# Kernel optimization log

Hardware: AMD Instinct MI355X
Metric: run time of the kernel (lower is better)

The kernel has to match this reference:

```python
import jax, jax.numpy as jnp
from jax import lax
import numpy as np

SCALE, K_UP = 2, 5


def conv2d(x, w, pad=0, dil=1):
    return lax.conv_general_dilated(x, w, (1, 1), [(pad, pad), (pad, pad)],
                                    rhs_dilation=(dil, dil),
                                    dimension_numbers=('NCHW', 'OIHW', 'NCHW'))


def cbr(x, w, g, b, pad=0, relu=True):
    # Conv (no bias) + BatchNorm (eval: running_mean=0, running_var=1, eps=1e-5) + optional ReLU
    x = conv2d(x, w, pad)
    x = x * (g / jnp.sqrt(1.0 + 1e-5))[None, :, None, None] + b[None, :, None, None]
    return jnp.maximum(x, 0.0) if relu else x


def resize_bilinear_ac(x, ho, wo):
    # bilinear interpolation, align_corners=True (matches F.interpolate)
    B, C, H, W = x.shape
    ys = jnp.linspace(0.0, H - 1.0, ho)
    xs = jnp.linspace(0.0, W - 1.0, wo)
    y0 = jnp.floor(ys).astype(jnp.int32); y1 = jnp.minimum(y0 + 1, H - 1)
    x0 = jnp.floor(xs).astype(jnp.int32); x1 = jnp.minimum(x0 + 1, W - 1)
    wy = (ys - y0).astype(x.dtype)
    wx = (xs - x0).astype(x.dtype)
    top = x[:, :, y0, :]
    bot = x[:, :, y1, :]
    v = top * (1.0 - wy)[None, None, :, None] + bot * wy[None, None, :, None]
    return v[:, :, :, x0] * (1.0 - wx) + v[:, :, :, x1] * wx


def setup_inputs() -> dict:
    key = jax.random.key(0)
    ks = jax.random.split(key, 10)
    B, CH, CL, H, W = 4, 256, 128, 64, 64
    CMID, CO, IC, KENC = 64, 128, 64, 3

    def wgt(k, shape):
        fan = int(np.prod(shape[1:]))
        return (jax.random.normal(k, shape, jnp.float32) / np.sqrt(fan)).astype(jnp.float32)

    d = {}
    d['x_h'] = jax.random.normal(ks[0], (B, CH, H, W), jnp.float32)
    d['x_l'] = jax.random.normal(ks[1], (B, CL, H * SCALE, W * SCALE), jnp.float32)
    d['w_reduce'] = wgt(ks[2], (IC, CH, 3, 3)); d['g_reduce'] = jnp.ones(IC); d['b_reduce'] = jnp.zeros(IC)
    d['w1'] = wgt(ks[3], (CMID, CH, 1, 1)); d['g1'] = jnp.ones(CMID); d['b1'] = jnp.zeros(CMID)
    d['w2'] = wgt(ks[4], (CMID, CL, 1, 1)); d['g2'] = jnp.ones(CMID); d['b2'] = jnp.zeros(CMID)
    d['w_enc'] = wgt(ks[5], (K_UP * K_UP, 2 * CMID, KENC, KENC)); d['g_enc'] = jnp.ones(K_UP * K_UP); d['b_enc'] = jnp.zeros(K_UP * K_UP)
    d['w_out1'] = wgt(ks[6], (CO, IC + CL, 3, 3)); d['g_out1'] = jnp.ones(CO); d['b_out1'] = jnp.zeros(CO)
    d['w_out2'] = wgt(ks[7], (CO, CO, 1, 1)); d['g_out2'] = jnp.ones(CO); d['b_out2'] = jnp.zeros(CO)
    return d


def reference(x_h, x_l, w_reduce, g_reduce, b_reduce, w1, g1, b1, w2, g2, b2,
              w_enc, g_enc, b_enc, w_out1, g_out1, b_out1, w_out2, g_out2, b_out2):
    b, c, h, w = x_h.shape
    h_, w_ = h * SCALE, w * SCALE
    # content encoder -> per-pixel reassembly kernels
    x1 = resize_bilinear_ac(cbr(x_h, w1, g1, b1), h_, w_)          # [b, cmid, h_, w_]
    x2 = cbr(x_l, w2, g2, b2)                                       # [b, cmid, h_, w_]
    Wm = cbr(jnp.concatenate([x1, x2], axis=1), w_enc, g_enc, b_enc, pad=1, relu=False)
    Wm = jax.nn.softmax(Wm, axis=1)                                  # [b, k_up^2, h_, w_]
    # reduced high-level features, upsampled
    xr = cbr(x_h, w_reduce, g_reduce, b_reduce, pad=1)               # [b, ic, h, w]
    xu = resize_bilinear_ac(xr, h_, w_)                              # [b, ic, h_, w_]
    # CARAFE-style reassembly: unfold(k=5, dilation=2, pad=4) expressed as
    # 25 shifted windows of the zero-padded map -> no k^2-blown buffer.
    pad = (K_UP // 2) * SCALE
    xp = jnp.pad(xu, ((0, 0), (0, 0), (pad, pad), (pad, pad)))
    X = jnp.zeros_like(xu)
    for i in range(K_UP):
        for j in range(K_UP):
            win = xp[:, :, i * SCALE:i * SCALE + h_, j * SCALE:j * SCALE + w_]
            X = X + Wm[:, i * K_UP + j][:, None] * win
    y = jnp.concatenate([X, x_l], axis=1)
    y = cbr(y, w_out1, g_out1, b_out1, pad=1)
    y = cbr(y, w_out2, g_out2, b_out2)
    return y
```

## Files before the change

### kernel.cpp

```cpp
#include <hip/hip_runtime.h>
#include <math.h>

#define BNS 0.99999500003749981f

typedef short          bf16x8  __attribute__((ext_vector_type(8)));
typedef float          f32x4   __attribute__((ext_vector_type(4)));
typedef unsigned short u16x8   __attribute__((ext_vector_type(8)));
typedef unsigned short u16x4   __attribute__((ext_vector_type(4)));
typedef unsigned short ushort_t;

__device__ inline ushort_t f2b(float f) {
    union { float f; unsigned int u; } x; x.f = f;
    unsigned int u = x.u;
    unsigned int r = (u + 0x7FFFu + ((u >> 16) & 1u)) >> 16;
    return (ushort_t)r;
}
__device__ inline float b2f(ushort_t s) {
    union { unsigned int u; float f; } x; x.u = ((unsigned int)s) << 16;
    return x.f;
}

__device__ inline void glds16(const ushort_t* gp, void* lp) {
    __builtin_amdgcn_global_load_lds(
        (const __attribute__((address_space(1))) unsigned int*)gp,
        (__attribute__((address_space(3))) unsigned int*)lp, 16, 0, 0);
}

template<int N, bool LG0>
__device__ __forceinline__ void wait_v() {
    if constexpr (LG0) {
        if constexpr (N == 0) asm volatile("s_waitcnt vmcnt(0) lgkmcnt(0)" ::: "memory");
        if constexpr (N == 3) asm volatile("s_waitcnt vmcnt(3) lgkmcnt(0)" ::: "memory");
        if constexpr (N == 4) asm volatile("s_waitcnt vmcnt(4) lgkmcnt(0)" ::: "memory");
        if constexpr (N == 5) asm volatile("s_waitcnt vmcnt(5) lgkmcnt(0)" ::: "memory");
        if constexpr (N == 6) asm volatile("s_waitcnt vmcnt(6) lgkmcnt(0)" ::: "memory");
    } else {
        if constexpr (N == 0) asm volatile("s_waitcnt vmcnt(0)" ::: "memory");
        if constexpr (N == 3) asm volatile("s_waitcnt vmcnt(3)" ::: "memory");
        if constexpr (N == 4) asm volatile("s_waitcnt vmcnt(4)" ::: "memory");
        if constexpr (N == 5) asm volatile("s_waitcnt vmcnt(5)" ::: "memory");
        if constexpr (N == 6) asm volatile("s_waitcnt vmcnt(6)" ::: "memory");
    }
}

#define E_BWR   0u
#define E_BW1   147456u
#define E_BW2   163840u
#define E_BWE   172032u
#define E_BWO1  208896u
#define E_BWO2  430080u
#define E_ZP    446464u
#define OFF_R1  524288u
#define OFF_R4  4718592u
#define OFF_R2  8912896u
#define OFF_R3  9961472u
#define OFF_R6  11010048u
#define OFF_R5  13107200u


__device__ inline void wseg3(int idx, const float* src, ushort_t* dst,
                             int TAPS, int COT, int CIT, int CO_real) {
    int kt  = idx / (COT * 32);
    int r   = idx - kt * (COT * 32);
    int q   = r / (COT * 8);
    int r2  = r - q * (COT * 8);
    int co  = r2 >> 3;
    int e   = r2 & 7;
    int KCT = CIT >> 5;
    int tap = kt / KCT, j = kt - tap * KCT;
    int ci  = j * 32 + q * 8 + e;
    float v = (co < CO_real) ? src[((size_t)co * CIT + ci) * TAPS + tap] : 0.f;
    dst[idx] = f2b(v);
}

__global__ __launch_bounds__(256)
void prep_weights(const float* wr, const float* w1, const float* w2,
                  const float* we, const float* wo1, const float* wo2,
                  ushort_t* ws0)
{
    int idx = blockIdx.x * 256 + threadIdx.x;
    const int n0 = 9*64*256;
    const int n1 = 64*256;
    const int n2 = 64*128;
    const int n3 = 9*32*128;
    const int n4 = 9*128*192;
    const int n5 = 128*128;
    if (idx < n0) { wseg3(idx, wr,  ws0 + E_BWR,  9, 64, 256, 64);  return; } idx -= n0;
    if (idx < n1) { wseg3(idx, w1,  ws0 + E_BW1,  1, 64, 256, 64);  return; } idx -= n1;
    if (idx < n2) { wseg3(idx, w2,  ws0 + E_BW2,  1, 64, 128, 64);  return; } idx -= n2;
    if (idx < n3) { wseg3(idx, we,  ws0 + E_BWE,  9, 32, 128, 25);  return; } idx -= n3;
    if (idx < n4) { wseg3(idx, wo1, ws0 + E_BWO1, 9, 128, 192, 128); return; } idx -= n4;
    if (idx < n5) { wseg3(idx, wo2, ws0 + E_BWO2, 1, 128, 128, 128); return; } idx -= n5;
    if (idx < 32768) ws0[E_ZP + idx] = 0;
}

__global__ __launch_bounds__(256)
void nchw2t16(const float* __restrict__ in, ushort_t* __restrict__ out,
              int C, int LHW, int npx)
{
    int px = blockIdx.x * 256 + threadIdx.x;
    if (px >= npx) return;
    int HW = 1 << LHW;
    int b = px >> LHW, phw = px & (HW - 1);
    const float* src = in + (size_t)b * C * HW + phw;
    unsigned base = (unsigned)(px >> 4) * (C * 16) + (unsigned)(px & 15) * 8;
    for (int c0 = 0; c0 < C; c0 += 8) {
        u16x8 o;
#pragma unroll
        for (int j = 0; j < 8; j++) o[j] = f2b(src[(size_t)(c0 + j) * HW]);
        *reinterpret_cast<u16x8*>(out + base + (c0 >> 3) * 128) = o;
    }
}

template<int TAPS, int BM, int CIA, int CIB, int COT, int BN, int G, int EPI>
__global__ __launch_bounds__(256)
void conv_lds(const ushort_t* __restrict__ ws0,
              unsigned offA, unsigned offB, unsigned offW,
              const float* __restrict__ g, const float* __restrict__ bia,
              int COclamp, void* __restrict__ outp,
              int H, int LHW, int relu)
{
    constexpr int KCA = CIA / 32, KCB = CIB / 32;
    constexpr int KCT = KCA + KCB;
    constexpr int NW  = (TAPS == 9) ? 3 : G;
    constexpr int ACP = (TAPS == 9) ? 1 : G;
    constexpr int NPH = (TAPS == 9) ? 3 * KCT : KCT / G;
    constexpr int MF = BM / 32, NF = BN / 32;
    constexpr int ACHUNK = BM / 16;
    constexpr int A4 = ACP * ACHUNK / 4;
    constexpr int WUNIT = BN / 16;
    constexpr int TWU = NW * WUNIT;
    constexpr int W4 = (TWU + 3) / 4;
    constexpr int SS = A4 + W4;
    constexpr int WOFF = ACP * BM * 64;
    constexpr int ZS   = WOFF + NW * BN * 64;
    constexpr int BUF  = ZS + 16;
    constexpr int LBN3 = (BN == 128) ? 10 : (BN == 64) ? 9 : 8;
    __shared__ __align__(16) char lds[2 * BUF];

    const unsigned nx = gridDim.x, ox = blockIdx.x;
    const unsigned qq = nx >> 3, xcd = ox & 7, k0 = ox >> 3;
    const unsigned bx = xcd * qq + k0;
    const int co_blk = blockIdx.y * BN;

    const int tid = threadIdx.x, w = tid >> 6, lane = tid & 63;
    const int l15 = lane & 15, lhi = lane >> 4;
    const int wpx = (w & 1) * (BM / 2), cw0 = (w >> 1) * (BN / 2);
    const int yb = (int)(bx & (unsigned)(H - 1));
    const unsigned pxc0 = bx * ACHUNK;

    if (tid < 8) *(unsigned*)(lds + (tid >> 2) * BUF + ZS + (tid & 3) * 4) = 0u;

    int aA[3][MF];
#pragma unroll
    for (int dxi = 0; dxi < 3; ++dxi) {
        const int dx = dxi - 1;
#pragma unroll
        for (int mf = 0; mf < MF; ++mf) {
            int pr = wpx + mf * 16 + l15 + dx;
            bool ok = (TAPS == 1) ? true : (pr >= 0 && pr < BM);
            aA[dxi][mf] = ok ? (((pr >> 4) << 10) + (lhi << 8) + ((pr & 15) << 4))
                             : (ZS - ((TAPS == 9) ? 0 : 0));
            if (TAPS == 9 && !ok) aA[dxi][mf] = ZS;
        }
    }
    int wA[NF];
#pragma unroll
    for (int nf = 0; nf < NF; ++nf)
        wA[nf] = (lhi * BN + cw0 + nf * 16 + l15) * 16;

    f32x4 acc[NF][MF];
#pragma unroll
    for (int nf = 0; nf < NF; ++nf)
#pragma unroll
        for (int mf = 0; mf < MF; ++mf)
            acc[nf][mf] = (f32x4){0.f, 0.f, 0.f, 0.f};

    auto stage = [&](int p, int bsel) {
        char* lb = lds + bsel * BUF;
        if constexpr (TAPS == 9) {
            const int dyi = p / KCT, kc = p - dyi * KCT;
            const int dy = dyi - 1;
            const bool isA = (kc < KCA);
            const int kcs = isA ? kc : kc - KCA;
            const int CI  = isA ? CIA : CIB;
            const unsigned offS = isA ? offA : offB;
            const bool rowv = (yb + dy >= 0) && (yb + dy < H);
#pragma unroll
            for (int i = 0; i < A4; ++i) {
                int u = i * 4 + w;
                unsigned s = rowv
                    ? offS + (unsigned)((int)pxc0 + dy * ACHUNK + u) * (unsigned)(CI * 16)
                           + (unsigned)(kcs * 512) + (unsigned)(lane * 8)
                    : E_ZP + (unsigned)(lane * 8);
                glds16(ws0 + s, lb + u * 1024);
            }
#pragma unroll
            for (int i = 0; i < W4; ++i) {
                int t3 = (i * 4 + w) % TWU;
                int tl = t3 / WUNIT, uu = t3 - tl * WUNIT;
                unsigned wsrc = offW + (unsigned)((dyi * 3 + tl) * KCT + kc)
                                       * (unsigned)(COT * 32);
                int el  = uu * 512 + lane * 8;
                int q   = el >> LBN3;
                int col = (el & ((1 << LBN3) - 1)) >> 3;
                glds16(ws0 + wsrc + q * (COT * 8) + (co_blk + col) * 8,
                       lb + WOFF + tl * (BN * 64) + uu * 1024);
            }
        } else {
#pragma unroll
            for (int i = 0; i < A4; ++i) {
                int lin = i * 4 + w;
                int gc = lin / ACHUNK, u = lin - gc * ACHUNK;
                unsigned s = offA + (unsigned)(pxc0 + u) * (unsigned)(CIA * 16)
                           + (unsigned)((p * G + gc) * 512) + (unsigned)(lane * 8);
                glds16(ws0 + s, lb + gc * (BM * 64) + u * 1024);
            }
#pragma unroll
            for (int i = 0; i < W4; ++i) {
                int t3 = (i * 4 + w) % TWU;
                int tl = t3 / WUNIT, uu = t3 - tl * WUNIT;
                unsigned wsrc = offW + (unsigned)(p * G + tl) * (unsigned)(COT * 32);
                int el  = uu * 512 + lane * 8;
                int q   = el >> LBN3;
                int col = (el & ((1 << LBN3) - 1)) >> 3;
                glds16(ws0 + wsrc + q * (COT * 8) + (co_blk + col) * 8,
                       lb + WOFF + tl * (BN * 64) + uu * 1024);
            }
        }
    };

    auto step = [&](int p, int bsel) {
        const char* lb = lds + bsel * BUF;
#pragma unroll
        for (int t = 0; t < NW; ++t) {
            const int dxi = (TAPS == 9) ? t : 1;
            const char* ab = lb + ((TAPS == 9) ? 0 : t * (BM * 64));
            bf16x8 af[MF], wf[NF];
#pragma unroll
            for (int mf = 0; mf < MF; ++mf)
                af[mf] = *reinterpret_cast<const bf16x8*>(ab + aA[dxi][mf]);
#pragma unroll
            for (int nf = 0; nf < NF; ++nf)
                wf[nf] = *reinterpret_cast<const bf16x8*>(
                    lb + WOFF + t * (BN * 64) + wA[nf]);
#pragma unroll
            for (int nf = 0; nf < NF; ++nf)
#pragma unroll
                for (int mf = 0; mf < MF; ++mf)
                    acc[nf][mf] = __builtin_amdgcn_mfma_f32_16x16x32_bf16(
                        wf[nf], af[mf], acc[nf][mf], 0, 0, 0);
        }
    };

    stage(0, 0);
#pragma unroll
    for (int p = 0; p < NPH; ++p) {
        if (p + 1 < NPH) stage(p + 1, (p + 1) & 1);
        if (p == 0) { if (p + 1 < NPH) wait_v<SS, true >(); else wait_v<0, true >(); }
        else        { if (p + 1 < NPH) wait_v<SS, false>(); else wait_v<0, false>(); }
        __builtin_amdgcn_s_barrier();
        __builtin_amdgcn_sched_barrier(0);
        step(p, p & 1);
        __builtin_amdgcn_sched_barrier(0);
        if (p + 1 < NPH) __builtin_amdgcn_s_barrier();
    }

    if constexpr (EPI == 0) {
        ushort_t* o1 = (ushort_t*)outp;
#pragma unroll
        for (int nf = 0; nf < NF; ++nf) {
            const int cg = co_blk + cw0 + nf * 16 + (lhi << 2);
            float sc[4], bi[4];
#pragma unroll
            for (int r = 0; r < 4; r++) {
                int c = min(cg + r, COclamp - 1);
                sc[r] = g[c] * BNS; bi[r] = bia[c];
            }
#pragma unroll
            for (int mf = 0; mf < MF; ++mf) {
                f32x4 a = acc[nf][mf];
                u16x4 ov;
#pragma unroll
                for (int r = 0; r < 4; r++) {
                    float v = fmaf(a[r], sc[r], bi[r]);
                    if (relu) v = fmaxf(v, 0.f);
                    ov[r] = f2b(v);
                }
                int px = (int)bx * BM + wpx + mf * 16 + l15;
                unsigned off = (unsigned)(px >> 4) * (COT * 16)
                             + (unsigned)(cg >> 3) * 128
                             + (unsigned)(px & 15) * 8 + (unsigned)(cg & 7);
                *reinterpret_cast<u16x4*>(o1 + off) = ov;
            }
        }
    } else if constexpr (EPI == 1) {
        float* o1 = (float*)outp;
        const int HW = 1 << LHW;
#pragma unroll
        for (int nf = 0; nf < NF; ++nf) {
            const int cg = co_blk + cw0 + nf * 16 + (lhi << 2);
            float sc[4], bi[4];
#pragma unroll
            for (int r = 0; r < 4; r++) {
                int c = min(cg + r, COclamp - 1);
                sc[r] = g[c] * BNS; bi[r] = bia[c];
            }
#pragma unroll
            for (int mf = 0; mf < MF; ++mf) {
                int px = (int)bx * BM + wpx + mf * 16 + l15;
                int b = px >> LHW, phw = px & (HW - 1);
#pragma unroll
                for (int r = 0; r < 4; r++) {
                    float v = fmaf(acc[nf][mf][r], sc[r], bi[r]);
                    if (relu) v = fmaxf(v, 0.f);
                    o1[((size_t)(b * COT + cg + r)) * HW + phw] = v;
                }
            }
        }
    } else {
        __syncthreads();
        float* sf = (float*)lds;
#pragma unroll
        for (int mf = 0; mf < MF; ++mf) {
            const int cg = cw0 + (lhi << 2);
            int pxl = wpx + mf * 16 + l15;
            f32x4 a = acc[0][mf];
#pragma unroll
            for (int r = 0; r < 4; r++) {
                int c = min(cg + r, COclamp - 1);
                sf[(cg + r) * 136 + pxl] = fmaf(a[r], g[c] * BNS, bia[c]);
            }
        }
        __syncthreads();
        if (tid < BM) {
            int gpx = (int)bx * BM + tid;
            float v[25];
#pragma unroll
            for (int c = 0; c < 25; ++c) v[c] = sf[c * 136 + tid];
            float m = v[0];
#pragma unroll
            for (int c = 1; c < 25; ++c) m = fmaxf(m, v[c]);
            float s = 0.f;
#pragma unroll
            for (int c = 0; c < 25; ++c) { v[c] = __expf(v[c] - m); s += v[c]; }
            float inv = 1.f / s;
            ushort_t* o1 = (ushort_t*)outp;
            unsigned base = (unsigned)(gpx >> 4) * (COT * 16) + (unsigned)(gpx & 15) * 8;
#pragma unroll
            for (int q = 0; q < 3; ++q) {
                u16x8 ov;
#pragma unroll
                for (int k = 0; k < 8; k++) ov[k] = f2b(v[q * 8 + k] * inv);
                *reinterpret_cast<u16x8*>(o1 + base + q * 128) = ov;
            }
            o1[base + 384] = f2b(v[24] * inv);
        }
    }
}

__global__ __launch_bounds__(256)
void resize2x_t16(const ushort_t* __restrict__ in, ushort_t* __restrict__ out)
{
    int t = blockIdx.x * 256 + threadIdx.x;
    int cg = t & 7;
    int opx = t >> 3;
    int xo = opx & 127;
    int rest = opx >> 7;
    int yo = rest & 127;
    int b  = rest >> 7;
    float fy = (float)yo * 63.f / 127.f;
    float fx = (float)xo * 63.f / 127.f;
    int y0 = (int)fy, x0 = (int)fx;
    float wy = fy - (float)y0, wx = fx - (float)x0;
    int y1 = min(y0 + 1, 63), x1 = min(x0 + 1, 63);
    int qb = b * 4096;
#define RD(Y, X) (*reinterpret_cast<const bf16x8*>(in + \
    (unsigned)(((qb + (Y) * 64 + (X)) >> 4) * 1024) + cg * 128 + ((qb + (Y) * 64 + (X)) & 15) * 8))
    bf16x8 v00 = RD(y0, x0), v01 = RD(y0, x1), v10 = RD(y1, x0), v11 = RD(y1, x1);
#undef RD
    u16x8 o;
#pragma unroll
    for (int k = 0; k < 8; k++) {
        float l = b2f((ushort_t)v00[k]) * (1.f - wy) + b2f((ushort_t)v10[k]) * wy;
        float r = b2f((ushort_t)v01[k]) * (1.f - wy) + b2f((ushort_t)v11[k]) * wy;
        o[k] = f2b(l * (1.f - wx) + r * wx);
    }
    *reinterpret_cast<u16x8*>(out + (unsigned)(opx >> 4) * 1024 + cg * 128 + (opx & 15) * 8) = o;
}

__global__ __launch_bounds__(256)
void carafe25(const ushort_t* __restrict__ wm, const ushort_t* __restrict__ xu,
              ushort_t* __restrict__ out)
{
    int t = blockIdx.x * 256 + threadIdx.x;
    int cg = t & 7;
    int px = t >> 3;
    int x = px & 127;
    int y = (px >> 7) & 127;
    const ushort_t* wp = wm + (unsigned)(px >> 4) * 512 + (px & 15) * 8;
    u16x8 r0 = *reinterpret_cast<const u16x8*>(wp);
    u16x8 r1 = *reinterpret_cast<const u16x8*>(wp + 128);
    u16x8 r2 = *reinterpret_cast<const u16x8*>(wp + 256);
    float v[25];
#pragma unroll
    for (int k = 0; k < 8; k++) v[k]      = b2f(r0[k]);
#pragma unroll
    for (int k = 0; k < 8; k++) v[8 + k]  = b2f(r1[k]);
#pragma unroll
    for (int k = 0; k < 8; k++) v[16 + k] = b2f(r2[k]);
    v[24] = b2f(wp[384]);

    float acc[8];
#pragma unroll
    for (int k = 0; k < 8; k++) acc[k] = 0.f;
#pragma unroll
    for (int i = 0; i < 5; i++) {
        int yy = y + 2 * i - 4;
#pragma unroll
        for (int j = 0; j < 5; j++) {
            int xx = x + 2 * j - 4;
            if (yy >= 0 && yy < 128 && xx >= 0 && xx < 128) {
                int q = px + (2 * i - 4) * 128 + (2 * j - 4);
                bf16x8 xv = *reinterpret_cast<const bf16x8*>(
                    xu + (unsigned)(q >> 4) * 1024 + cg * 128 + (q & 15) * 8);
                float wv = v[i * 5 + j];
#pragma unroll
                for (int k = 0; k < 8; k++)
                    acc[k] = fmaf(wv, b2f((ushort_t)xv[k]), acc[k]);
            }
        }
    }
    u16x8 o;
#pragma unroll
    for (int k = 0; k < 8; k++) o[k] = f2b(acc[k]);
    *reinterpret_cast<u16x8*>(out + (unsigned)(px >> 4) * 1024 + cg * 128 + (px & 15) * 8) = o;
}

extern "C" void kernel_launch(void* const* d_in, const int* in_sizes, int n_in,
                              void* d_out, int out_size, void* d_ws, size_t ws_size,
                              hipStream_t stream)
{
    const float* x_h      = (const float*)d_in[0];
    const float* x_l      = (const float*)d_in[1];
    const float* w_reduce = (const float*)d_in[2];
    const float* g_reduce = (const float*)d_in[3];
    const float* b_reduce = (const float*)d_in[4];
    const float* w1       = (const float*)d_in[5];
    const float* g1       = (const float*)d_in[6];
    const float* b1       = (const float*)d_in[7];
    const float* w2       = (const float*)d_in[8];
    const float* g2       = (const float*)d_in[9];
    const float* b2       = (const float*)d_in[10];
    const float* w_enc    = (const float*)d_in[11];
    const float* g_enc    = (const float*)d_in[12];
    const float* b_enc    = (const float*)d_in[13];
    const float* w_out1   = (const float*)d_in[14];
    const float* g_out1   = (const float*)d_in[15];
    const float* b_out1   = (const float*)d_in[16];
    const float* w_out2   = (const float*)d_in[17];
    const float* g_out2   = (const float*)d_in[18];
    const float* b_out2   = (const float*)d_in[19];

    ushort_t* ws0 = (ushort_t*)d_ws;

    const unsigned oXHC = OFF_R1;
    const unsigned oC1  = OFF_R2;
    const unsigned oXR  = OFF_R3;
    const unsigned oX1  = OFF_R4;
    const unsigned oXLC = OFF_R5;
    const unsigned oX2  = OFF_R1;
    const unsigned oWM  = OFF_R6;
    const unsigned oXU  = OFF_R4;
    const unsigned oXB  = OFF_R1;
    const unsigned oY1  = OFF_R4;

    prep_weights<<<1872, 256, 0, stream>>>(w_reduce, w1, w2, w_enc, w_out1, w_out2, ws0);
    nchw2t16<<<64, 256, 0, stream>>>(x_h, ws0 + oXHC, 256, 12, 16384);
    conv_lds<1, 64, 256, 0, 64, 32, 2, 0><<<dim3(256, 2), 256, 0, stream>>>(
        ws0, oXHC, 0u, E_BW1, g1, b1, 64, ws0 + oC1, 64, 12, 1);
    conv_lds<9, 64, 256, 0, 64, 32, 1, 0><<<dim3(256, 2), 256, 0, stream>>>(
        ws0, oXHC, 0u, E_BWR, g_reduce, b_reduce, 64, ws0 + oXR, 64, 12, 1);
    resize2x_t16<<<2048, 256, 0, stream>>>(ws0 + oC1, ws0 + oX1);
    nchw2t16<<<256, 256, 0, stream>>>(x_l, ws0 + oXLC, 128, 14, 65536);
    conv_lds<1, 128, 128, 0, 64, 32, 2, 0><<<dim3(512, 2), 256, 0, stream>>>(
        ws0, oXLC, 0u, E_BW2, g2, b2, 64, ws0 + oX2, 128, 14, 1);
    conv_lds<9, 128, 64, 64, 32, 32, 1, 2><<<dim3(512, 1), 256, 0, stream>>>(
        ws0, oX1, oX2, E_BWE, g_enc, b_enc, 25, ws0 + oWM, 128, 14, 0);
    resize2x_t16<<<2048, 256, 0, stream>>>(ws0 + oXR, ws0 + oXU);
    carafe25<<<2048, 256, 0, stream>>>(ws0 + oWM, ws0 + oXU, ws0 + oXB);
    conv_lds<9, 128, 64, 128, 128, 64, 1, 0><<<dim3(512, 2), 256, 0, stream>>>(
        ws0, oXB, oXLC, E_BWO1, g_out1, b_out1, 128, ws0 + oY1, 128, 14, 1);
    conv_lds<1, 128, 128, 0, 128, 64, 2, 1><<<dim3(512, 2), 256, 0, stream>>>(
        ws0, oY1, 0u, E_BWO2, g_out2, b_out2, 128, d_out, 128, 14, 1);
}
```

Measured before the change: 155.4 us.

## Merge prep kernels, widen conv output tiles, add 3-stage pipeline and MFMA priority

Fuses the weight-prep kernel and both NCHW-to-tiled input conversion kernels into one launch. Generalizes the conv kernel's wave layout (WSX) so a block covers all output channels (BN 64/128, grid.y = 1), which stops input tiles being loaded twice. Adds an optional 3-deep LDS pipeline with matching vmcnt waits, and raises wave priority around the MFMA loop. The cost is more LDS and registers per block, which may lower occupancy, and half as many blocks on some convs.

After: 135.6 us. -12.7%, faster.

```diff
diff --git a/kernel.cpp b/kernel.cpp
--- a/kernel.cpp
+++ b/kernel.cpp
@@ -28,18 +28,19 @@
 
 template<int N, bool LG0>
 __device__ __forceinline__ void wait_v() {
+    static_assert(N >= 0 && N <= 16, "vmcnt literal table");
     if constexpr (LG0) {
-        if constexpr (N == 0) asm volatile("s_waitcnt vmcnt(0) lgkmcnt(0)" ::: "memory");
-        if constexpr (N == 3) asm volatile("s_waitcnt vmcnt(3) lgkmcnt(0)" ::: "memory");
-        if constexpr (N == 4) asm volatile("s_waitcnt vmcnt(4) lgkmcnt(0)" ::: "memory");
-        if constexpr (N == 5) asm volatile("s_waitcnt vmcnt(5) lgkmcnt(0)" ::: "memory");
-        if constexpr (N == 6) asm volatile("s_waitcnt vmcnt(6) lgkmcnt(0)" ::: "memory");
+        if constexpr (N == 0)  asm volatile("s_waitcnt vmcnt(0) lgkmcnt(0)" ::: "memory");
+        if constexpr (N == 3)  asm volatile("s_waitcnt vmcnt(3) lgkmcnt(0)" ::: "memory");
+        if constexpr (N == 4)  asm volatile("s_waitcnt vmcnt(4) lgkmcnt(0)" ::: "memory");
+        if constexpr (N == 6)  asm volatile("s_waitcnt vmcnt(6) lgkmcnt(0)" ::: "memory");
+        if constexpr (N == 8)  asm volatile("s_waitcnt vmcnt(8) lgkmcnt(0)" ::: "memory");
     } else {
-        if constexpr (N == 0) asm volatile("s_waitcnt vmcnt(0)" ::: "memory");
-        if constexpr (N == 3) asm volatile("s_waitcnt vmcnt(3)" ::: "memory");
-        if constexpr (N == 4) asm volatile("s_waitcnt vmcnt(4)" ::: "memory");
-        if constexpr (N == 5) asm volatile("s_waitcnt vmcnt(5)" ::: "memory");
-        if constexpr (N == 6) asm volatile("s_waitcnt vmcnt(6)" ::: "memory");
+        if constexpr (N == 0)  asm volatile("s_waitcnt vmcnt(0)" ::: "memory");
+        if constexpr (N == 3)  asm volatile("s_waitcnt vmcnt(3)" ::: "memory");
+        if constexpr (N == 4)  asm volatile("s_waitcnt vmcnt(4)" ::: "memory");
+        if constexpr (N == 6)  asm volatile("s_waitcnt vmcnt(6)" ::: "memory");
+        if constexpr (N == 8)  asm volatile("s_waitcnt vmcnt(8)" ::: "memory");
     }
 }
 
@@ -73,32 +74,9 @@
     dst[idx] = f2b(v);
 }
 
-__global__ __launch_bounds__(256)
-void prep_weights(const float* wr, const float* w1, const float* w2,
-                  const float* we, const float* wo1, const float* wo2,
-                  ushort_t* ws0)
-{
-    int idx = blockIdx.x * 256 + threadIdx.x;
-    const int n0 = 9*64*256;
-    const int n1 = 64*256;
-    const int n2 = 64*128;
-    const int n3 = 9*32*128;
-    const int n4 = 9*128*192;
-    const int n5 = 128*128;
-    if (idx < n0) { wseg3(idx, wr,  ws0 + E_BWR,  9, 64, 256, 64);  return; } idx -= n0;
-    if (idx < n1) { wseg3(idx, w1,  ws0 + E_BW1,  1, 64, 256, 64);  return; } idx -= n1;
-    if (idx < n2) { wseg3(idx, w2,  ws0 + E_BW2,  1, 64, 128, 64);  return; } idx -= n2;
-    if (idx < n3) { wseg3(idx, we,  ws0 + E_BWE,  9, 32, 128, 25);  return; } idx -= n3;
-    if (idx < n4) { wseg3(idx, wo1, ws0 + E_BWO1, 9, 128, 192, 128); return; } idx -= n4;
-    if (idx < n5) { wseg3(idx, wo2, ws0 + E_BWO2, 1, 128, 128, 128); return; } idx -= n5;
-    if (idx < 32768) ws0[E_ZP + idx] = 0;
-}
-
-__global__ __launch_bounds__(256)
-void nchw2t16(const float* __restrict__ in, ushort_t* __restrict__ out,
-              int C, int LHW, int npx)
-{
-    int px = blockIdx.x * 256 + threadIdx.x;
+__device__ inline void cvt_t16(const float* __restrict__ in,
+                               ushort_t* __restrict__ out,
+                               int C, int LHW, int px, int npx) {
     if (px >= npx) return;
     int HW = 1 << LHW;
     int b = px >> LHW, phw = px & (HW - 1);
@@ -112,7 +90,38 @@
     }
 }
 
-template<int TAPS, int BM, int CIA, int CIB, int COT, int BN, int G, int EPI>
+__global__ __launch_bounds__(256)
+void prep_all(const float* wr, const float* w1, const float* w2,
+              const float* we, const float* wo1, const float* wo2,
+              const float* xh, const float* xl, ushort_t* ws0)
+{
+    int bx = blockIdx.x;
+    int tid = threadIdx.x;
+    if (bx < 1872) {
+        int idx = bx * 256 + tid;
+        const int n0 = 9*64*256;
+        const int n1 = 64*256;
+        const int n2 = 64*128;
+        const int n3 = 9*32*128;
+        const int n4 = 9*128*192;
+        const int n5 = 128*128;
+        if (idx < n0) { wseg3(idx, wr,  ws0 + E_BWR,  9, 64, 256, 64);  return; } idx -= n0;
+        if (idx < n1) { wseg3(idx, w1,  ws0 + E_BW1,  1, 64, 256, 64);  return; } idx -= n1;
+        if (idx < n2) { wseg3(idx, w2,  ws0 + E_BW2,  1, 64, 128, 64);  return; } idx -= n2;
+        if (idx < n3) { wseg3(idx, we,  ws0 + E_BWE,  9, 32, 128, 25);  return; } idx -= n3;
+        if (idx < n4) { wseg3(idx, wo1, ws0 + E_BWO1, 9, 128, 192, 128); return; } idx -= n4;
+        if (idx < n5) { wseg3(idx, wo2, ws0 + E_BWO2, 1, 128, 128, 128); return; } idx -= n5;
+        if (idx < 32768) ws0[E_ZP + idx] = 0;
+        return;
+    }
+    bx -= 1872;
+    if (bx < 64) { cvt_t16(xh, ws0 + OFF_R1, 256, 12, bx * 256 + tid, 16384); return; }
+    bx -= 64;
+    cvt_t16(xl, ws0 + OFF_R5, 128, 14, bx * 256 + tid, 65536);
+}
+
+template<int TAPS, int BM, int CIA, int CIB, int COT, int BN, int G,
+         int WSX, int DEP, int EPI>
 __global__ __launch_bounds__(256)
 void conv_lds(const ushort_t* __restrict__ ws0,
               unsigned offA, unsigned offB, unsigned offW,
@@ -125,9 +134,11 @@
     constexpr int NW  = (TAPS == 9) ? 3 : G;
     constexpr int ACP = (TAPS == 9) ? 1 : G;
     constexpr int NPH = (TAPS == 9) ? 3 * KCT : KCT / G;
-    constexpr int MF = BM / 32, NF = BN / 32;
+    constexpr int WSY = 4 / WSX;
+    constexpr int MF = BM / WSX / 16;
+    constexpr int NF = BN / WSY / 16;
     constexpr int ACHUNK = BM / 16;
-    constexpr int A4 = ACP * ACHUNK / 4;
+    constexpr int A4 = (ACP * ACHUNK + 3) / 4;
     constexpr int WUNIT = BN / 16;
     constexpr int TWU = NW * WUNIT;
     constexpr int W4 = (TWU + 3) / 4;
@@ -136,7 +147,7 @@
     constexpr int ZS   = WOFF + NW * BN * 64;
     constexpr int BUF  = ZS + 16;
     constexpr int LBN3 = (BN == 128) ? 10 : (BN == 64) ? 9 : 8;
-    __shared__ __align__(16) char lds[2 * BUF];
+    __shared__ __align__(16) char lds[DEP * BUF];
 
     const unsigned nx = gridDim.x, ox = blockIdx.x;
     const unsigned qq = nx >> 3, xcd = ox & 7, k0 = ox >> 3;
@@ -145,11 +156,12 @@
 
     const int tid = threadIdx.x, w = tid >> 6, lane = tid & 63;
     const int l15 = lane & 15, lhi = lane >> 4;
-    const int wpx = (w & 1) * (BM / 2), cw0 = (w >> 1) * (BN / 2);
+    const int wpx = (w % WSX) * (BM / WSX);
+    const int cw0 = (w / WSX) * (BN / WSY);
     const int yb = (int)(bx & (unsigned)(H - 1));
     const unsigned pxc0 = bx * ACHUNK;
 
-    if (tid < 8) *(unsigned*)(lds + (tid >> 2) * BUF + ZS + (tid & 3) * 4) = 0u;
+    if (tid < 4 * DEP) *(unsigned*)(lds + (tid >> 2) * BUF + ZS + (tid & 3) * 4) = 0u;
 
     int aA[3][MF];
 #pragma unroll
@@ -159,9 +171,7 @@
         for (int mf = 0; mf < MF; ++mf) {
             int pr = wpx + mf * 16 + l15 + dx;
             bool ok = (TAPS == 1) ? true : (pr >= 0 && pr < BM);
-            aA[dxi][mf] = ok ? (((pr >> 4) << 10) + (lhi << 8) + ((pr & 15) << 4))
-                             : (ZS - ((TAPS == 9) ? 0 : 0));
-            if (TAPS == 9 && !ok) aA[dxi][mf] = ZS;
+            aA[dxi][mf] = ok ? (((pr >> 4) << 10) + (lhi << 8) + ((pr & 15) << 4)) : ZS;
         }
     }
     int wA[NF];
@@ -188,7 +198,7 @@
             const bool rowv = (yb + dy >= 0) && (yb + dy < H);
 #pragma unroll
             for (int i = 0; i < A4; ++i) {
-                int u = i * 4 + w;
+                int u = (i * 4 + w) % ACHUNK;
                 unsigned s = rowv
                     ? offS + (unsigned)((int)pxc0 + dy * ACHUNK + u) * (unsigned)(CI * 16)
                            + (unsigned)(kcs * 512) + (unsigned)(lane * 8)
@@ -210,7 +220,7 @@
         } else {
 #pragma unroll
             for (int i = 0; i < A4; ++i) {
-                int lin = i * 4 + w;
+                int lin = (i * 4 + w) % (ACP * ACHUNK);
                 int gc = lin / ACHUNK, u = lin - gc * ACHUNK;
                 unsigned s = offA + (unsigned)(pxc0 + u) * (unsigned)(CIA * 16)
                            + (unsigned)((p * G + gc) * 512) + (unsigned)(lane * 8);
@@ -232,6 +242,7 @@
 
     auto step = [&](int p, int bsel) {
         const char* lb = lds + bsel * BUF;
+        __builtin_amdgcn_s_setprio(1);
 #pragma unroll
         for (int t = 0; t < NW; ++t) {
             const int dxi = (TAPS == 9) ? t : 1;
@@ -251,17 +262,31 @@
                     acc[nf][mf] = __builtin_amdgcn_mfma_f32_16x16x32_bf16(
                         wf[nf], af[mf], acc[nf][mf], 0, 0, 0);
         }
+        __builtin_amdgcn_s_setprio(0);
     };
 
     stage(0, 0);
+    if constexpr (DEP == 3) { if (1 < NPH) stage(1, 1); }
 #pragma unroll
     for (int p = 0; p < NPH; ++p) {
-        if (p + 1 < NPH) stage(p + 1, (p + 1) & 1);
-        if (p == 0) { if (p + 1 < NPH) wait_v<SS, true >(); else wait_v<0, true >(); }
-        else        { if (p + 1 < NPH) wait_v<SS, false>(); else wait_v<0, false>(); }
+        if (p + DEP - 1 < NPH) stage(p + DEP - 1, (p + DEP - 1) % DEP);
+        if constexpr (DEP == 3) {
+            if (p == 0) {
+                if (p + 2 < NPH)      wait_v<2 * SS, true >();
+                else if (p + 1 < NPH) wait_v<SS,     true >();
+                else                  wait_v<0,      true >();
+            } else {
+                if (p + 2 < NPH)      wait_v<2 * SS, false>();
+                else if (p + 1 < NPH) wait_v<SS,     false>();
+                else                  wait_v<0,      false>();
+            }
+        } else {
+            if (p == 0) { if (p + 1 < NPH) wait_v<SS, true >(); else wait_v<0, true >(); }
+            else        { if (p + 1 < NPH) wait_v<SS, false>(); else wait_v<0, false>(); }
+        }
         __builtin_amdgcn_s_barrier();
         __builtin_amdgcn_sched_barrier(0);
-        step(p, p & 1);
+        step(p, p % DEP);
         __builtin_amdgcn_sched_barrier(0);
         if (p + 1 < NPH) __builtin_amdgcn_s_barrier();
     }
@@ -322,14 +347,17 @@
         __syncthreads();
         float* sf = (float*)lds;
 #pragma unroll
-        for (int mf = 0; mf < MF; ++mf) {
-            const int cg = cw0 + (lhi << 2);
-            int pxl = wpx + mf * 16 + l15;
-            f32x4 a = acc[0][mf];
-#pragma unroll
-            for (int r = 0; r < 4; r++) {
-                int c = min(cg + r, COclamp - 1);
-                sf[(cg + r) * 136 + pxl] = fmaf(a[r], g[c] * BNS, bia[c]);
+        for (int nf = 0; nf < NF; ++nf) {
+            const int cg = cw0 + nf * 16 + (lhi << 2);
+#pragma unroll
+            for (int mf = 0; mf < MF; ++mf) {
+                int pxl = wpx + mf * 16 + l15;
+                f32x4 a = acc[nf][mf];
+#pragma unroll
+                for (int r = 0; r < 4; r++) {
+                    int c = min(cg + r, COclamp - 1);
+                    sf[(cg + r) * 136 + pxl] = fmaf(a[r], g[c] * BNS, bia[c]);
+                }
             }
         }
         __syncthreads();
@@ -346,7 +374,7 @@
             for (int c = 0; c < 25; ++c) { v[c] = __expf(v[c] - m); s += v[c]; }
             float inv = 1.f / s;
             ushort_t* o1 = (ushort_t*)outp;
-            unsigned base = (unsigned)(gpx >> 4) * (COT * 16) + (unsigned)(gpx & 15) * 8;
+            unsigned base = (unsigned)(gpx >> 4) * (32 * 16) + (unsigned)(gpx & 15) * 8;
 #pragma unroll
             for (int q = 0; q < 3; ++q) {
                 u16x8 ov;
@@ -475,22 +503,21 @@
     const unsigned oXB  = OFF_R1;
     const unsigned oY1  = OFF_R4;
 
-    prep_weights<<<1872, 256, 0, stream>>>(w_reduce, w1, w2, w_enc, w_out1, w_out2, ws0);
-    nchw2t16<<<64, 256, 0, stream>>>(x_h, ws0 + oXHC, 256, 12, 16384);
-    conv_lds<1, 64, 256, 0, 64, 32, 2, 0><<<dim3(256, 2), 256, 0, stream>>>(
+    prep_all<<<2192, 256, 0, stream>>>(w_reduce, w1, w2, w_enc, w_out1, w_out2,
+                                       x_h, x_l, ws0);
+    conv_lds<1, 64, 256, 0, 64, 64, 2, 2, 3, 0><<<dim3(256, 1), 256, 0, stream>>>(
         ws0, oXHC, 0u, E_BW1, g1, b1, 64, ws0 + oC1, 64, 12, 1);
-    conv_lds<9, 64, 256, 0, 64, 32, 1, 0><<<dim3(256, 2), 256, 0, stream>>>(
+    conv_lds<9, 64, 256, 0, 64, 64, 1, 2, 3, 0><<<dim3(256, 1), 256, 0, stream>>>(
         ws0, oXHC, 0u, E_BWR, g_reduce, b_reduce, 64, ws0 + oXR, 64, 12, 1);
     resize2x_t16<<<2048, 256, 0, stream>>>(ws0 + oC1, ws0 + oX1);
-    nchw2t16<<<256, 256, 0, stream>>>(x_l, ws0 + oXLC, 128, 14, 65536);
-    conv_lds<1, 128, 128, 0, 64, 32, 2, 0><<<dim3(512, 2), 256, 0, stream>>>(
+    conv_lds<1, 128, 128, 0, 64, 64, 1, 2, 3, 0><<<dim3(512, 1), 256, 0, stream>>>(
         ws0, oXLC, 0u, E_BW2, g2, b2, 64, ws0 + oX2, 128, 14, 1);
-    conv_lds<9, 128, 64, 64, 32, 32, 1, 2><<<dim3(512, 1), 256, 0, stream>>>(
+    conv_lds<9, 128, 64, 64, 32, 32, 1, 4, 3, 2><<<dim3(512, 1), 256, 0, stream>>>(
         ws0, oX1, oX2, E_BWE, g_enc, b_enc, 25, ws0 + oWM, 128, 14, 0);
     resize2x_t16<<<2048, 256, 0, stream>>>(ws0 + oXR, ws0 + oXU);
     carafe25<<<2048, 256, 0, stream>>>(ws0 + oWM, ws0 + oXU, ws0 + oXB);
-    conv_lds<9, 128, 64, 128, 128, 64, 1, 0><<<dim3(512, 2), 256, 0, stream>>>(
+    conv_lds<9, 128, 64, 128, 128, 128, 1, 2, 2, 0><<<dim3(512, 1), 256, 0, stream>>>(
         ws0, oXB, oXLC, E_BWO1, g_out1, b_out1, 128, ws0 + oY1, 128, 14, 1);
-    conv_lds<1, 128, 128, 0, 128, 64, 2, 1><<<dim3(512, 2), 256, 0, stream>>>(
+    conv_lds<1, 128, 128, 0, 128, 128, 2, 2, 2, 1><<<dim3(512, 1), 256, 0, stream>>>(
         ws0, oY1, 0u, E_BWO2, g_out2, b_out2, 128, d_out, 128, 14, 1);
 }
```
